# Kernel optimization log

Hardware: AMD Instinct MI355X
Metric: run time of the kernel (lower is better)

Reference implementation:

```python
import jax, jax.numpy as jnp
import numpy as np

EMBED = 256; DEPTH = 64; DEPTH_START = 1.0
POS_RANGE = (-61.2, -61.2, -10.0, 61.2, 61.2, 10.0)
PC_RANGE = (-51.2, -51.2, -5.0, 51.2, 51.2, 3.0)
MEM_LEN = 512; TOPK = 256; NUM_Q = 900; NUM_CLS = 10; CODE = 10; L = 6
B, N, H, W = 4, 6, 16, 44
PAD_H, PAD_W = 256, 704
TWO_PI = 2.0 * np.pi


def _posemb(coords, nf=128):
    # sine/cosine embedding per coordinate channel -> [..., C, nf]
    dim_t = 10000.0 ** (2.0 * (jnp.arange(nf, dtype=jnp.float32) // 2) / nf)
    p = (coords * TWO_PI)[..., None] / dim_t
    p = jnp.stack([jnp.sin(p[..., 0::2]), jnp.cos(p[..., 1::2])], -1)
    return p.reshape(p.shape[:-2] + (nf,))


def _mlp2(x, W1, b1, W2, b2):
    return jnp.maximum(x @ W1 + b1, 0.0) @ W2 + b2


def _conv1x1(x, Wt, b):
    return jnp.einsum('bchw,co->bohw', x, Wt) + b[None, :, None, None]


def _ln(x, g, b):
    m = jnp.mean(x, -1, keepdims=True)
    v = jnp.mean(jnp.square(x - m), -1, keepdims=True)
    return (x - m) / jnp.sqrt(v + 1e-5) * g + b


def _sine_pe(not_mask):
    # SinePositionalEncoding2D, normalize=True; not_mask: [BN,H,W] float
    nf = EMBED // 2; eps = 1e-6
    y = jnp.cumsum(not_mask, 1); x = jnp.cumsum(not_mask, 2)
    y = y / (y[:, -1:, :] + eps) * TWO_PI
    x = x / (x[:, :, -1:] + eps) * TWO_PI
    dim_t = 10000.0 ** (2.0 * (jnp.arange(nf, dtype=jnp.float32) // 2) / nf)
    px = x[..., None] / dim_t; py = y[..., None] / dim_t
    px = jnp.stack([jnp.sin(px[..., 0::2]), jnp.cos(px[..., 1::2])], -1).reshape(x.shape + (nf,))
    py = jnp.stack([jnp.sin(py[..., 0::2]), jnp.cos(py[..., 1::2])], -1).reshape(y.shape + (nf,))
    return jnp.concatenate([py, px], -1).transpose(0, 3, 1, 2)  # [BN,EMBED,H,W]


def _forward(feat, lidar2img, prev_exists, memory_embedding, memory_reference_point,
             memory_timestamp, outs_dec, ref_pts, ip_w, ip_b, pe_w1, pe_b1, pe_w2, pe_b2,
             ap_w1, ap_b1, ap_w2, ap_b2, qe_w1, qe_b1, qe_w2, qe_b2, te_w1, te_b1, te_w2,
             te_b2, cls_w1, cls_b1, cls_g1, cls_be1, cls_w2, cls_b2, cls_g2, cls_be2,
             cls_w3, cls_b3, reg_w1, reg_b1, reg_w2, reg_b2, reg_w3, reg_b3, masks):
    b, n, c, h, w = feat.shape
    # --- pre_update_memory: memory_refresh + timestamp advance ---
    prev = prev_exists.reshape(b, 1, 1)
    mem_e = memory_embedding * prev
    mem_r = memory_reference_point * prev
    mem_t = memory_timestamp * prev + prev
    # --- input projection (1x1 conv) ---
    x = _conv1x1(feat.reshape(b * n, c, h, w), ip_w, ip_b).reshape(b, n, EMBED, h, w)
    # --- 3D position embedding (PETR frustum) ---
    coords_h = jnp.arange(h, dtype=jnp.float32) * (float(PAD_H) / h)
    coords_w = jnp.arange(w, dtype=jnp.float32) * (float(PAD_W) / w)
    d = jnp.arange(DEPTH, dtype=jnp.float32)
    bin_size = (POS_RANGE[3] - DEPTH_START) / (DEPTH * (1.0 + DEPTH))
    coords_d = DEPTH_START + bin_size * d * (d + 1.0)  # LID discretization
    cw, ch_, cd = jnp.meshgrid(coords_w, coords_h, coords_d, indexing='ij')  # [W,H,D]
    xy = jnp.stack([cw, ch_], -1) * jnp.maximum(cd, 1e-5)[..., None]
    coords4 = jnp.concatenate([xy, cd[..., None], jnp.ones_like(cd[..., None])], -1)  # [W,H,D,4]
    img2lidars = jnp.linalg.inv(lidar2img)  # [B,N,4,4]
    c3 = jnp.einsum('bnij,whdj->bnwhdi', img2lidars, coords4)[..., :3]  # [B,N,W,H,D,3]
    lo = jnp.asarray(POS_RANGE[:3], jnp.float32); hi = jnp.asarray(POS_RANGE[3:], jnp.float32)
    c3 = (c3 - lo) / (hi - lo)
    cmask = ((c3 > 1.0) | (c3 < 0.0)).reshape(b, n, w, h, DEPTH * 3).sum(-1) > DEPTH * 0.5
    coords_mask = masks | cmask.transpose(0, 1, 3, 2)
    c3 = c3.transpose(0, 1, 4, 5, 3, 2).reshape(b * n, DEPTH * 3, h, w)
    c3 = jnp.clip(c3, 0.0, 1.0)
    c3 = jnp.log(jnp.clip(c3, 1e-5, None) / jnp.clip(1.0 - c3, 1e-5, None))  # inverse_sigmoid
    coords_pos = _conv1x1(jnp.maximum(_conv1x1(c3, pe_w1, pe_b1), 0.0), pe_w2, pe_b2)
    coords_pos = coords_pos.reshape(b, n, EMBED, h, w)
    # --- 2D sine PE + adapt_pos3d ---
    sine = _sine_pe((~masks).astype(jnp.float32).reshape(b * n, h, w))
    sine = _conv1x1(jnp.maximum(_conv1x1(sine, ap_w1, ap_b1), 0.0), ap_w2, ap_b2)
    pos_embed = coords_pos + sine.reshape(b, n, EMBED, h, w)
    # --- query / time embeddings ---
    qp = _posemb(ref_pts)  # [Q,3,128]
    qp = jnp.concatenate([qp[:, 1], qp[:, 0], qp[:, 2]], -1)  # (y,x,z) -> [Q,384]
    query_pos = _mlp2(qp, qe_w1, qe_b1, qe_w2, qe_b2)  # [Q,256]
    tp = _posemb(mem_t)[..., 0, :]  # [B,M,128]
    time_emb = _mlp2(tp, te_w1, te_b1, te_w2, te_b2)  # [B,M,256]
    # --- cls / reg branches, stacked over decoder layers ---
    hc = jnp.maximum(_ln(jnp.einsum('lbqd,lde->lbqe', outs_dec, cls_w1) + cls_b1[:, None, None], cls_g1[:, None, None], cls_be1[:, None, None]), 0.0)
    hc = jnp.maximum(_ln(jnp.einsum('lbqd,lde->lbqe', hc, cls_w2) + cls_b2[:, None, None], cls_g2[:, None, None], cls_be2[:, None, None]), 0.0)
    all_cls = jnp.einsum('lbqd,ldc->lbqc', hc, cls_w3) + cls_b3[:, None, None]
    hr = jnp.maximum(jnp.einsum('lbqd,lde->lbqe', outs_dec, reg_w1) + reg_b1[:, None, None], 0.0)
    hr = jnp.maximum(jnp.einsum('lbqd,lde->lbqe', hr, reg_w2) + reg_b2[:, None, None], 0.0)
    all_reg = jnp.einsum('lbqd,ldc->lbqc', hr, reg_w3) + reg_b3[:, None, None]
    # --- post_update_memory: sigmoid + topk + gather + rolling concat ---
    rec_score = jnp.max(jax.nn.sigmoid(all_cls[-1]), -1)  # topk(1) over classes == max
    _, idx = jax.lax.top_k(rec_score, TOPK)  # [B,K]
    rec_mem = jax.lax.stop_gradient(jnp.take_along_axis(outs_dec[-1], idx[..., None], axis=1))
    rec_ref = jax.lax.stop_gradient(jnp.take_along_axis(all_reg[-1][..., :3], idx[..., None], axis=1))
    pmin = jnp.asarray(PC_RANGE[:3], jnp.float32); pmax = jnp.asarray(PC_RANGE[3:], jnp.float32)
    rec_ref = jnp.clip((rec_ref - pmin) / jnp.clip(pmax - pmin, 1e-5, None), 0.0, 1.0)
    rec_ts = jnp.zeros((b, TOPK, 1), rec_mem.dtype)
    new_mem_e = jnp.concatenate([rec_mem, mem_e], 1)[:, :MEM_LEN]
    new_mem_r = jnp.concatenate([rec_ref, mem_r], 1)[:, :MEM_LEN]
    new_mem_t = jnp.concatenate([rec_ts, mem_t], 1)[:, :MEM_LEN]
    return (all_cls, all_reg, new_mem_e, new_mem_r, new_mem_t, pos_embed, x, query_pos, time_emb, coords_mask)


def setup_inputs() -> dict:
    key = jax.random.key(0)
    ks = jax.random.split(key, 24)
    def rn(k, shape, s=0.02):
        return jax.random.normal(k, shape, jnp.float32) * s
    inp = dict(
        feat=jax.random.normal(ks[0], (B, N, 256, H, W), jnp.float32),
        lidar2img=jnp.eye(4, dtype=jnp.float32) + 0.05 * jax.random.normal(ks[1], (B, N, 4, 4), jnp.float32),
        prev_exists=jnp.array([1.0, 0.0, 1.0, 1.0], jnp.float32),
        memory_embedding=jax.random.normal(ks[2], (B, MEM_LEN, EMBED), jnp.float32),
        memory_reference_point=jax.random.uniform(ks[3], (B, MEM_LEN, 3)),
        memory_timestamp=jax.random.uniform(ks[4], (B, MEM_LEN, 1)),
        outs_dec=jax.random.normal(ks[5], (L, B, NUM_Q, EMBED), jnp.float32),
        ref_pts=jax.random.uniform(ks[6], (NUM_Q, 3)),
        ip_w=rn(ks[7], (256, EMBED)), ip_b=jnp.zeros(EMBED),
        pe_w1=rn(ks[8], (3 * DEPTH, EMBED * 2)), pe_b1=jnp.zeros(EMBED * 2),
        pe_w2=rn(ks[9], (EMBED * 2, EMBED)), pe_b2=jnp.zeros(EMBED),
        ap_w1=rn(ks[10], (EMBED, EMBED)), ap_b1=jnp.zeros(EMBED),
        ap_w2=rn(ks[11], (EMBED, EMBED)), ap_b2=jnp.zeros(EMBED),
        qe_w1=rn(ks[12], (EMBED * 3 // 2, EMBED)), qe_b1=jnp.zeros(EMBED),
        qe_w2=rn(ks[13], (EMBED, EMBED)), qe_b2=jnp.zeros(EMBED),
        te_w1=rn(ks[14], (EMBED // 2, EMBED)), te_b1=jnp.zeros(EMBED),
        te_w2=rn(ks[15], (EMBED, EMBED)), te_b2=jnp.zeros(EMBED),
        cls_w1=rn(ks[16], (L, EMBED, EMBED)), cls_b1=jnp.zeros((L, EMBED)),
        cls_g1=jnp.ones((L, EMBED)), cls_be1=jnp.zeros((L, EMBED)),
        cls_w2=rn(ks[17], (L, EMBED, EMBED)), cls_b2=jnp.zeros((L, EMBED)),
        cls_g2=jnp.ones((L, EMBED)), cls_be2=jnp.zeros((L, EMBED)),
        cls_w3=rn(ks[18], (L, EMBED, NUM_CLS)), cls_b3=jnp.zeros((L, NUM_CLS)),
        reg_w1=rn(ks[19], (L, EMBED, EMBED)), reg_b1=jnp.zeros((L, EMBED)),
        reg_w2=rn(ks[20], (L, EMBED, EMBED)), reg_b2=jnp.zeros((L, EMBED)),
        reg_w3=rn(ks[21], (L, EMBED, CODE)), reg_b3=jnp.zeros((L, CODE)),
        masks=jnp.zeros((B, N, H, W), bool),
    )
    return inp


def reference(feat, lidar2img, prev_exists, memory_embedding, memory_reference_point,
              memory_timestamp, outs_dec, ref_pts, ip_w, ip_b, pe_w1, pe_b1, pe_w2, pe_b2,
              ap_w1, ap_b1, ap_w2, ap_b2, qe_w1, qe_b1, qe_w2, qe_b2, te_w1, te_b1, te_w2,
              te_b2, cls_w1, cls_b1, cls_g1, cls_be1, cls_w2, cls_b2, cls_g2, cls_be2,
              cls_w3, cls_b3, reg_w1, reg_b1, reg_w2, reg_b2, reg_w3, reg_b3, masks):
    return _forward(feat, lidar2img, prev_exists, memory_embedding, memory_reference_point,
                    memory_timestamp, outs_dec, ref_pts, ip_w, ip_b, pe_w1, pe_b1, pe_w2, pe_b2,
                    ap_w1, ap_b1, ap_w2, ap_b2, qe_w1, qe_b1, qe_w2, qe_b2, te_w1, te_b1, te_w2,
                    te_b2, cls_w1, cls_b1, cls_g1, cls_be1, cls_w2, cls_b2, cls_g2, cls_be2,
                    cls_w3, cls_b3, reg_w1, reg_b1, reg_w2, reg_b2, reg_w3, reg_b3, masks)
```

## Files before the change

### kernel.cpp

```cpp
#include <hip/hip_runtime.h>
#include <math.h>


typedef unsigned short u16;
typedef __attribute__((ext_vector_type(8))) short short8v;
typedef __attribute__((ext_vector_type(4))) float f32x4;

#define DI __device__ __forceinline__
DI u16 f2bf(float f) {
    unsigned x = __float_as_uint(f);
    return (u16)((x + 0x7fffu + ((x >> 16) & 1u)) >> 16);
}
DI float bf2f(u16 u) { return __uint_as_float(((unsigned)u) << 16); }

#define TWO_PI_F 6.283185307179586f

__global__ __launch_bounds__(256) void k_pesrc(
    const float* __restrict__ l2i, u16* __restrict__ c3aT, float* __restrict__ cm,
    float* __restrict__ sineb) {
    int bid = blockIdx.x, tid = threadIdx.x;
    if (bid < 4224) {
        int pix = bid * 4 + (tid >> 6);
        int d = tid & 63;
        int bn = pix / 704, p = pix - bn * 704;
        int h = p / 44, w = p - h * 44;
        const float* Ms = l2i + bn * 16;
        float a[4][8];
#pragma unroll
        for (int i = 0; i < 4; i++)
#pragma unroll
            for (int j = 0; j < 4; j++) {
                a[i][j] = Ms[i * 4 + j];
                a[i][4 + j] = (i == j) ? 1.f : 0.f;
            }
#pragma unroll
        for (int c = 0; c < 4; c++) {
            float ip = 1.f / a[c][c];
#pragma unroll
            for (int j = 0; j < 8; j++) a[c][j] *= ip;
#pragma unroll
            for (int r = 0; r < 4; r++) {
                if (r == c) continue;
                float f = a[r][c];
#pragma unroll
                for (int j = 0; j < 8; j++) a[r][j] -= f * a[c][j];
            }
        }
        float cw = w * 16.0f, ch = h * 16.0f;
        const float bin = (61.2f - 1.0f) / (64.0f * 65.0f);
        float cd = 1.0f + (bin * d) * (d + 1.0f);
        float xx = cw * cd, yy = ch * cd;
        float px = a[0][4] * xx + a[0][5] * yy + a[0][6] * cd + a[0][7];
        float py = a[1][4] * xx + a[1][5] * yy + a[1][6] * cd + a[1][7];
        float pz = a[2][4] * xx + a[2][5] * yy + a[2][6] * cd + a[2][7];
        float c[3];
        c[0] = (px + 61.2f) * (1.f / 122.4f);
        c[1] = (py + 61.2f) * (1.f / 122.4f);
        c[2] = (pz + 10.0f) * (1.f / 20.0f);
        u16* o = c3aT + (size_t)pix * 192 + d * 3;
        int cnt = 0;
#pragma unroll
        for (int i = 0; i < 3; i++) {
            cnt += ((c[i] > 1.0f) || (c[i] < 0.0f)) ? 1 : 0;
            float cc = fminf(fmaxf(c[i], 0.f), 1.f);
            float num = fmaxf(cc, 1e-5f);
            float den = fmaxf(1.0f - cc, 1e-5f);
            o[i] = f2bf(logf(num / den));
        }
        for (int off = 32; off; off >>= 1) cnt += __shfl_down(cnt, off);
        if (d == 0) cm[pix] = (cnt > 32) ? 1.f : 0.f;
    } else {
        int idx = (bid - 4224) * 256 + tid;
        if (idx >= 256 * 704) return;
        int c = idx / 704, p = idx - c * 704;
        int h = p / 44, w = p - h * 44;
        float pos = (c < 128) ? (h + 1) * (TWO_PI_F / (16.0f + 1e-6f))
                              : (w + 1) * (TWO_PI_F / (44.0f + 1e-6f));
        int cc = c & 127, k = cc >> 1;
        float dt = powf(10000.f, k * (1.f / 64.f));
        float arg = pos / dt;
        sineb[idx] = (cc & 1) ? cosf(arg) : sinf(arg);
    }
}

__global__ __launch_bounds__(256) void k_tail(
    const float* __restrict__ memt, const float* __restrict__ prev,
    const float* __restrict__ rp,
    float* __restrict__ fin_t, float* __restrict__ fin_q,
    const float* __restrict__ me, const float* __restrict__ mr,
    float* __restrict__ oe, float* __restrict__ orr, float* __restrict__ ot) {
    int bid = blockIdx.x, tid = threadIdx.x;
    if (bid < 1187) {
        int idx = bid * 256 + tid;
        if (idx < 131072) {
            int row = idx >> 6, p = idx & 63;
            float pv = prev[row >> 9];
            float mt = memt[row] * pv + pv;
            float dt = powf(10000.f, p * (1.f / 64.f));
            float arg = mt * TWO_PI_F / dt;
            float s, c;
            sincosf(arg, &s, &c);
            *(float2*)&fin_t[row * 128 + 2 * p] = make_float2(s, c);
        } else if (idx < 131072 + 172800) {
            int q = idx - 131072;
            int row = q / 192, p = q - row * 192;
            int f = 2 * p, seg = f >> 7, ff = f & 127;
            int cidx = (seg == 0) ? 1 : ((seg == 1) ? 0 : 2);
            float rv = rp[row * 3 + cidx];
            float dt = powf(10000.f, (ff >> 1) * (1.f / 64.f));
            float arg = rv * TWO_PI_F / dt;
            float s, c;
            sincosf(arg, &s, &c);
            *(float2*)&fin_q[row * 384 + f] = make_float2(s, c);
        }
    } else {
        int bb = bid - 1187;
        int b = bb >> 8, j = bb & 255, o = tid;
        float pv = prev[b];
        oe[(size_t)(b * 512 + 256 + j) * 256 + o] = me[(size_t)(b * 512 + j) * 256 + o] * pv;
        if (o < 3)
            orr[(size_t)(b * 512 + 256 + j) * 3 + o] = mr[(size_t)(b * 512 + j) * 3 + o] * pv;
        if (o == 0) {
            ot[b * 512 + 256 + j] = memt[b * 512 + j] * pv + pv;
            ot[b * 512 + j] = 0.f;
        }
    }
}

__global__ __launch_bounds__(256) void k_wtrA(
    const float* __restrict__ cls_w1, const float* __restrict__ reg_w1,
    const float* __restrict__ cls_w2, const float* __restrict__ reg_w2,
    u16* __restrict__ w1Tc, u16* __restrict__ w1Tr,
    u16* __restrict__ w2Tc, u16* __restrict__ w2Tr,
    const float* __restrict__ pe_w1, u16* __restrict__ pe1T,
    const float* __restrict__ pe_w2, u16* __restrict__ pe2T,
    const float* __restrict__ ip_w, u16* __restrict__ ipT,
    const float* __restrict__ ap_w1, u16* __restrict__ ap1T,
    const float* __restrict__ ap_w2, u16* __restrict__ ap2T,
    const float* __restrict__ cls_w3, u16* __restrict__ c3T,
    const float* __restrict__ reg_w3, u16* __restrict__ r3T,
    const float* __restrict__ od, u16* __restrict__ odb) {
    __shared__ float sh[32][33];
    int bid = blockIdx.x;
    if (bid >= 2048) {
        int e0 = (bid - 2048) * 2048 + threadIdx.x * 8;
        int zz = e0 / 921600, rem = e0 - zz * 921600;
        int row = rem >> 8, c = rem & 255;
        const float* src = od + e0;
        float4 f0 = *(const float4*)src;
        float4 f1 = *(const float4*)(src + 4);
        uint4 u;
        u.x = f2bf(f0.x) | ((unsigned)f2bf(f0.y) << 16);
        u.y = f2bf(f0.z) | ((unsigned)f2bf(f0.w) << 16);
        u.z = f2bf(f1.x) | ((unsigned)f2bf(f1.y) << 16);
        u.w = f2bf(f1.z) | ((unsigned)f2bf(f1.w) << 16);
        u16* dst = odb + (size_t)zz * 1867776 +
                   ((size_t)((row >> 6) * 8 + (c >> 5))) * 4096 + (row & 63) * 32 + (c & 31);
        *(uint4*)dst = u;
        return;
    }
    if (bid >= 1952) {
        int r = bid - 1952;
        int ti = r >> 3, k0 = (r & 7) * 32;
        const float* src = (ti < 6) ? cls_w3 + (size_t)ti * 2560
                                    : reg_w3 + (size_t)(ti - 6) * 2560;
        u16* dst = (ti < 6) ? c3T + (size_t)ti * 2560
                            : r3T + (size_t)(ti - 6) * 2560;
        for (int i = threadIdx.x; i < 320; i += 256) {
            int k = i / 10, n = i - (i / 10) * 10;
            dst[n * 256 + k0 + k] = f2bf(src[(size_t)(k0 + k) * 10 + n]);
        }
        return;
    }
    const float* src; u16* dst; int K, N, x, y;
    if (bid < 1536) {
        int x_ = bid & 7, y_ = (bid >> 3) & 7, z = bid >> 6;
        int ti = z / 6, zz = z - ti * 6;
        const float* s = (ti == 0) ? cls_w1 : (ti == 1) ? reg_w1 : (ti == 2) ? cls_w2 : reg_w2;
        u16* dd = (ti == 0) ? w1Tc : (ti == 1) ? w1Tr : (ti == 2) ? w2Tc : w2Tr;
        src = s + (size_t)zz * 65536; dst = dd + (size_t)zz * 65536;
        K = 256; N = 256; x = x_; y = y_;
    } else if (bid < 1632) {
        int r = bid - 1536; x = r & 15; y = r >> 4;
        src = pe_w1; dst = pe1T; K = 192; N = 512;
    } else if (bid < 1760) {
        int r = bid - 1632; x = r & 7; y = r >> 3;
        src = pe_w2; dst = pe2T; K = 512; N = 256;
    } else {
        int r = bid - 1760; x = r & 7; y = (r >> 3) & 7;
        int ti = r >> 6;
        src = (ti == 0) ? ip_w : (ti == 1) ? ap_w1 : ap_w2;
        dst = (ti == 0) ? ipT : (ti == 1) ? ap1T : ap2T;
        K = 256; N = 256;
    }
    int n0 = x * 32, k0 = y * 32;
    int tx = threadIdx.x & 31, ty = threadIdx.x >> 5;
#pragma unroll
    for (int r = 0; r < 4; r++)
        sh[ty + 8 * r][tx] = src[(size_t)(k0 + ty + 8 * r) * N + n0 + tx];
    __syncthreads();
#pragma unroll
    for (int r = 0; r < 4; r++)
        dst[(size_t)(n0 + ty + 8 * r) * K + k0 + tx] = f2bf(sh[tx][ty + 8 * r]);
}

template <int AF32, int BTRANS, int BF32, int OUTF32, int ADD, int BIASM, int APANEL>
__global__ __launch_bounds__(256) void k_mfma(
    const void* __restrict__ Av, const void* __restrict__ B1v, const void* __restrict__ B2v,
    const float* __restrict__ bias1, const float* __restrict__ bias2,
    const float* __restrict__ add, void* __restrict__ outv,
    int M, int N, int K, int lda, int ldb, int ldo,
    long aZ, long bZ, long biasZ, long oZ, int zsplit, int zrelu, int aFull, int zpair) {
    __shared__ __align__(16) u16 As[64][40];
    __shared__ __align__(16) u16 Bs[128][40];
    const int tid = threadIdx.x;
    const int z = blockIdx.z;
    const int half = zpair ? (z & 1) : ((z < zsplit) ? 0 : 1);
    const int zz = zpair ? (z >> 1) : (z - (half ? zsplit : 0));
    const int lz = zpair ? (half * zsplit + zz) : z;
    const void* Bv = half ? B2v : B1v;
    const float* bias = (half ? bias2 : bias1) + (size_t)zz * biasZ;
    const bool relu = zpair ? (half >= zrelu) : (z >= zrelu);
    const long aOff = (long)(aFull ? lz : zz) * aZ;
    const long bOff = (long)zz * bZ;
    const int m0 = blockIdx.y * 64, n0 = blockIdx.x * 128;
    const int wave = tid >> 6, lane = tid & 63, quad = lane >> 4, l16 = lane & 15;
    const int wm = (wave >> 1) * 32, wn = (wave & 1) * 64;
    const int ar = tid >> 2, ak = (tid & 3) << 3;
    const int br = tid & 127, bk = (tid >> 7) << 4;
    f32x4 acc[2][4] = {};

    float pAf[8]; uint4 pAu = make_uint4(0, 0, 0, 0);
    float pBf[16]; u16 pBh[16];
    uint4 pBu0 = make_uint4(0, 0, 0, 0), pBu1 = make_uint4(0, 0, 0, 0);

    auto loadA = [&](int kt) {
        if (APANEL) {
            const u16* ap = (const u16*)Av + aOff +
                            ((size_t)(m0 >> 6) * (K >> 5) + (kt >> 5)) * 4096 + tid * 8;
            pAu = *(const uint4*)ap;
        } else if (AF32) {
            int gm = m0 + ar;
#pragma unroll
            for (int q = 0; q < 8; q++) pAf[q] = 0.f;
            if (gm < M) {
                const float* ap = (const float*)Av + aOff + (size_t)gm * lda + kt + ak;
                float4 f0 = *(const float4*)ap;
                float4 f1 = *(const float4*)(ap + 4);
                pAf[0] = f0.x; pAf[1] = f0.y; pAf[2] = f0.z; pAf[3] = f0.w;
                pAf[4] = f1.x; pAf[5] = f1.y; pAf[6] = f1.z; pAf[7] = f1.w;
            }
        } else {
            int gm = m0 + ar;
            pAu = make_uint4(0, 0, 0, 0);
            if (gm < M)
                pAu = *(const uint4*)((const u16*)Av + aOff + (size_t)gm * lda + kt + ak);
        }
    };
    auto storeA = [&]() {
        if (AF32) {
            uint4 u;
            u.x = f2bf(pAf[0]) | ((unsigned)f2bf(pAf[1]) << 16);
            u.y = f2bf(pAf[2]) | ((unsigned)f2bf(pAf[3]) << 16);
            u.z = f2bf(pAf[4]) | ((unsigned)f2bf(pAf[5]) << 16);
            u.w = f2bf(pAf[6]) | ((unsigned)f2bf(pAf[7]) << 16);
            *(uint4*)&As[ar][ak] = u;
        } else {
            *(uint4*)&As[ar][ak] = pAu;
        }
    };
    auto loadB = [&](int kt) {
        int gn = n0 + br;
        if (!BTRANS) {
            pBu0 = make_uint4(0, 0, 0, 0);
            pBu1 = make_uint4(0, 0, 0, 0);
            if (gn < N) {
                const u16* bp = (const u16*)Bv + bOff + (size_t)gn * ldb + kt + bk;
                pBu0 = *(const uint4*)bp;
                pBu1 = *(const uint4*)(bp + 8);
            }
        } else if (BF32) {
#pragma unroll
            for (int kk = 0; kk < 16; kk++)
                pBf[kk] = (gn < N) ? ((const float*)Bv + bOff)[(size_t)(kt + bk + kk) * ldb + gn]
                                   : 0.f;
        } else {
#pragma unroll
            for (int kk = 0; kk < 16; kk++)
                pBh[kk] = (gn < N) ? ((const u16*)Bv + bOff)[(size_t)(kt + bk + kk) * ldb + gn]
                                   : (u16)0;
        }
    };
    auto storeB = [&]() {
        if (!BTRANS) {
            *(uint4*)&Bs[br][bk] = pBu0;
            *(uint4*)&Bs[br][bk + 8] = pBu1;
        } else {
            u16 t[16];
#pragma unroll
            for (int kk = 0; kk < 16; kk++) t[kk] = BF32 ? f2bf(pBf[kk]) : pBh[kk];
            uint4 u0, u1;
            u0.x = t[0] | ((unsigned)t[1] << 16);
            u0.y = t[2] | ((unsigned)t[3] << 16);
            u0.z = t[4] | ((unsigned)t[5] << 16);
            u0.w = t[6] | ((unsigned)t[7] << 16);
            u1.x = t[8] | ((unsigned)t[9] << 16);
            u1.y = t[10] | ((unsigned)t[11] << 16);
            u1.z = t[12] | ((unsigned)t[13] << 16);
            u1.w = t[14] | ((unsigned)t[15] << 16);
            *(uint4*)&Bs[br][bk] = u0;
            *(uint4*)&Bs[br][bk + 8] = u1;
        }
    };

    loadA(0); loadB(0);
    for (int kt = 0; kt < K; kt += 32) {
        storeA(); storeB();
        __syncthreads();
        if (kt + 32 < K) { loadA(kt + 32); loadB(kt + 32); }
        short8v af[2], bfr[4];
#pragma unroll
        for (int i = 0; i < 2; i++) af[i] = *(const short8v*)&As[wm + i * 16 + l16][quad * 8];
#pragma unroll
        for (int j = 0; j < 4; j++) bfr[j] = *(const short8v*)&Bs[wn + j * 16 + l16][quad * 8];
#pragma unroll
        for (int i = 0; i < 2; i++)
#pragma unroll
            for (int j = 0; j < 4; j++)
                acc[i][j] = __builtin_amdgcn_mfma_f32_16x16x32_bf16(af[i], bfr[j], acc[i][j], 0, 0, 0);
        __syncthreads();
    }

    float* outf = (float*)outv + (size_t)lz * oZ;
    u16* outh = (u16*)outv + (size_t)lz * oZ;
#pragma unroll
    for (int i = 0; i < 2; i++) {
#pragma unroll
        for (int r = 0; r < 4; r++) {
            int row = m0 + wm + i * 16 + quad * 4 + r;
            if (row >= M) continue;
#pragma unroll
            for (int j = 0; j < 4; j++) {
                int col = n0 + wn + j * 16 + l16;
                if (col >= N) continue;
                float v = acc[i][j][r] + (BIASM ? bias[row] : bias[col]);
                if (relu) v = fmaxf(v, 0.f);
                if (ADD) v += add[(size_t)row * ldo + col];
                if (OUTF32) outf[(size_t)row * ldo + col] = v;
                else        outh[(size_t)row * ldo + col] = f2bf(v);
            }
        }
    }
}

template <int RELU>
DI void sgemm_body(const float* __restrict__ A, const float* __restrict__ Bm,
                   const float* __restrict__ bias, float* __restrict__ out,
                   int M, int K, int lda) {
    __shared__ __align__(16) float As[16][68];
    __shared__ __align__(16) float Bs[16][68];
    const int tid = threadIdx.x;
    const int m0 = blockIdx.y * 64, n0 = blockIdx.x * 64;
    const int tm = tid >> 4, tn = tid & 15;
    const int kA = tid >> 4, mA = (tid << 2) & 63;
    const int mN = tid & 63, kq = tid >> 6;
    float acc[4][4] = {};
    for (int kt = 0; kt < K; kt += 16) {
        int gm = m0 + mN;
        float4 u = {0.f, 0.f, 0.f, 0.f};
        if (gm < M) u = *(const float4*)(A + (size_t)gm * lda + kt + (kq << 2));
        As[(kq << 2) + 0][mN] = u.x; As[(kq << 2) + 1][mN] = u.y;
        As[(kq << 2) + 2][mN] = u.z; As[(kq << 2) + 3][mN] = u.w;
        {
            float4 b = *(const float4*)(Bm + (size_t)(kt + kA) * 256 + n0 + mA);
            Bs[kA][mA + 0] = b.x; Bs[kA][mA + 1] = b.y;
            Bs[kA][mA + 2] = b.z; Bs[kA][mA + 3] = b.w;
        }
        __syncthreads();
#pragma unroll
        for (int k = 0; k < 16; k++) {
            const float4 av = *(const float4*)(&As[k][tm << 2]);
            const float4 bv = *(const float4*)(&Bs[k][tn << 2]);
            float ar[4] = {av.x, av.y, av.z, av.w};
            float br[4] = {bv.x, bv.y, bv.z, bv.w};
#pragma unroll
            for (int i = 0; i < 4; i++)
#pragma unroll
                for (int j = 0; j < 4; j++) acc[i][j] = fmaf(ar[i], br[j], acc[i][j]);
        }
        __syncthreads();
    }
#pragma unroll
    for (int i = 0; i < 4; i++) {
        int row = m0 + (tm << 2) + i;
        if (row >= M) continue;
        float4 o4;
        o4.x = acc[i][0] + bias[n0 + (tn << 2) + 0];
        o4.y = acc[i][1] + bias[n0 + (tn << 2) + 1];
        o4.z = acc[i][2] + bias[n0 + (tn << 2) + 2];
        o4.w = acc[i][3] + bias[n0 + (tn << 2) + 3];
        if (RELU) {
            o4.x = fmaxf(o4.x, 0.f); o4.y = fmaxf(o4.y, 0.f);
            o4.z = fmaxf(o4.z, 0.f); o4.w = fmaxf(o4.w, 0.f);
        }
        *(float4*)(out + (size_t)row * 256 + n0 + (tn << 2)) = o4;
    }
}

template <int RELU>
__global__ __launch_bounds__(256) void k_sgemm2(
    const float* __restrict__ A, const float* __restrict__ Bm,
    const float* __restrict__ bias, float* __restrict__ out,
    int M, int K, int lda) {
    sgemm_body<RELU>(A, Bm, bias, out, M, K, lda);
}

template <int RELU>
__global__ __launch_bounds__(256) void k_sgemm3(
    const float* __restrict__ A0, const float* __restrict__ B0,
    const float* __restrict__ b0, float* __restrict__ o0, int M0, int K0, int lda0,
    const float* __restrict__ A1, const float* __restrict__ B1,
    const float* __restrict__ b1, float* __restrict__ o1, int M1, int K1, int lda1) {
    const float* A; const float* Bm; const float* bias; float* out; int M, K, lda;
    if (blockIdx.z == 0) { A = A0; Bm = B0; bias = b0; out = o0; M = M0; K = K0; lda = lda0; }
    else                 { A = A1; Bm = B1; bias = b1; out = o1; M = M1; K = K1; lda = lda1; }
    if ((int)blockIdx.y * 64 >= M) return;
    sgemm_body<RELU>(A, Bm, bias, out, M, K, lda);
}

__global__ __launch_bounds__(256) void k_lnb(
    u16* __restrict__ buf, const float* __restrict__ g, const float* __restrict__ be) {
    int tid = threadIdx.x, wid = tid >> 6, lane = tid & 63;
    int row = blockIdx.x * 4 + wid;
    int l = row / 3600;
    size_t base = (size_t)row * 256 + lane;
    float v[4];
#pragma unroll
    for (int i = 0; i < 4; i++) v[i] = bf2f(buf[base + (i << 6)]);
    float s = v[0] + v[1] + v[2] + v[3];
    for (int off = 32; off; off >>= 1) s += __shfl_down(s, off);
    s = __shfl(s, 0);
    float mean = s * (1.f / 256.f);
    float d[4], q = 0.f;
#pragma unroll
    for (int i = 0; i < 4; i++) { d[i] = v[i] - mean; q += d[i] * d[i]; }
    for (int off = 32; off; off >>= 1) q += __shfl_down(q, off);
    q = __shfl(q, 0);
    float rstd = rsqrtf(q * (1.f / 256.f) + 1e-5f);
#pragma unroll
    for (int i = 0; i < 4; i++) {
        int c = lane + (i << 6);
        buf[base + (i << 6)] = f2bf(fmaxf(d[i] * rstd * g[l * 256 + c] + be[l * 256 + c], 0.f));
    }
}

__global__ __launch_bounds__(256) void k_ln5(
    float* __restrict__ buf, const float* __restrict__ g, const float* __restrict__ be) {
    int tid = threadIdx.x, wid = tid >> 6, lane = tid & 63;
    int row = blockIdx.x * 4 + wid;
    size_t base = (size_t)row * 256 + lane;
    float v[4];
#pragma unroll
    for (int i = 0; i < 4; i++) v[i] = buf[base + (i << 6)];
    float s = v[0] + v[1] + v[2] + v[3];
    for (int off = 32; off; off >>= 1) s += __shfl_down(s, off);
    s = __shfl(s, 0);
    float mean = s * (1.f / 256.f);
    float d[4], q = 0.f;
#pragma unroll
    for (int i = 0; i < 4; i++) { d[i] = v[i] - mean; q += d[i] * d[i]; }
    for (int off = 32; off; off >>= 1) q += __shfl_down(q, off);
    q = __shfl(q, 0);
    float rstd = rsqrtf(q * (1.f / 256.f) + 1e-5f);
#pragma unroll
    for (int i = 0; i < 4; i++) {
        int c = lane + (i << 6);
        buf[base + (i << 6)] = fmaxf(d[i] * rstd * g[c] + be[c], 0.f);
    }
}

__global__ __launch_bounds__(320) void k_score(
    const float* __restrict__ h2, const float* __restrict__ wc, const float* __restrict__ bc,
    float* __restrict__ score) {
    __shared__ float sh[32][256];
    __shared__ float clsv[32][10];
    int tb = blockIdx.x * 32, tid = threadIdx.x;
    for (int i = tid; i < 8192; i += 320) {
        int rr = i >> 8, k = i & 255;
        int tok = tb + rr;
        sh[rr][k] = (tok < 3600) ? h2[(size_t)tok * 256 + k] : 0.f;
    }
    __syncthreads();
    int tl = tid / 10, o = tid - tl * 10;
    const float* w = wc + 5 * 2560 + o;
    float ac = 0.f;
    for (int k = 0; k < 256; k++) ac += sh[tl][k] * w[k * 10];
    ac += bc[5 * 10 + o];
    int tok = tb + tl;
    if (tok < 3600) clsv[tl][o] = ac;
    __syncthreads();
    if (tid < 32 && tb + tid < 3600) {
        float m = clsv[tid][0];
#pragma unroll
        for (int c = 1; c < 10; c++) m = fmaxf(m, clsv[tid][c]);
        score[tb + tid] = m;
    }
}

__global__ __launch_bounds__(1024) void k_sel(
    const float* __restrict__ score, int* __restrict__ sel) {
    __shared__ float sc[900];
    int b = blockIdx.x, tid = threadIdx.x;
    for (int i = tid; i < 900; i += 1024) sc[i] = score[b * 900 + i];
    __syncthreads();
    if (tid < 900) {
        float s = sc[tid];
        int r = 0;
        for (int j = 0; j < 900; j++) {
            float sj = sc[j];
            r += ((sj > s) || (sj == s && j < tid)) ? 1 : 0;
        }
        if (r < 256) sel[b * 256 + r] = tid;
    }
}

__global__ __launch_bounds__(256) void k_gather(
    const int* __restrict__ sel, const float* __restrict__ oreg,
    const float* __restrict__ od, float* __restrict__ oe, float* __restrict__ orr) {
    int b = blockIdx.y;
    int r = blockIdx.x * 4 + (threadIdx.x >> 6);
    int lane = threadIdx.x & 63;
    int q = sel[b * 256 + r];
    const float4* src = (const float4*)(od + (size_t)((20 + b) * 900 + q) * 256);
    float4* dst = (float4*)(oe + (size_t)(b * 512 + r) * 256);
    dst[lane] = src[lane];
    if (lane == 0) {
#pragma unroll
        for (int kk = 0; kk < 3; kk++) {
            float v = oreg[(size_t)(5 * 3600 + b * 900 + q) * 10 + kk];
            float lo = (kk == 2) ? -5.0f : -51.2f;
            float rng = (kk == 2) ? 8.0f : 102.4f;
            orr[(size_t)(b * 512 + r) * 3 + kk] = fminf(fmaxf((v - lo) / rng, 0.f), 1.f);
        }
    }
}

extern "C" void kernel_launch(void* const* d_in, const int* in_sizes, int n_in,
                              void* d_out, int out_size, void* d_ws, size_t ws_size,
                              hipStream_t stream) {
    const float* feat   = (const float*)d_in[0];
    const float* l2i    = (const float*)d_in[1];
    const float* prev   = (const float*)d_in[2];
    const float* meme   = (const float*)d_in[3];
    const float* memr   = (const float*)d_in[4];
    const float* memt   = (const float*)d_in[5];
    const float* od     = (const float*)d_in[6];
    const float* rp     = (const float*)d_in[7];
    const float* ip_w   = (const float*)d_in[8];
    const float* ip_b   = (const float*)d_in[9];
    const float* pe_w1  = (const float*)d_in[10];
    const float* pe_b1  = (const float*)d_in[11];
    const float* pe_w2  = (const float*)d_in[12];
    const float* pe_b2  = (const float*)d_in[13];
    const float* ap_w1  = (const float*)d_in[14];
    const float* ap_b1  = (const float*)d_in[15];
    const float* ap_w2  = (const float*)d_in[16];
    const float* ap_b2  = (const float*)d_in[17];
    const float* qe_w1  = (const float*)d_in[18];
    const float* qe_b1  = (const float*)d_in[19];
    const float* qe_w2  = (const float*)d_in[20];
    const float* qe_b2  = (const float*)d_in[21];
    const float* te_w1  = (const float*)d_in[22];
    const float* te_b1  = (const float*)d_in[23];
    const float* te_w2  = (const float*)d_in[24];
    const float* te_b2  = (const float*)d_in[25];
    const float* cls_w1 = (const float*)d_in[26];
    const float* cls_b1 = (const float*)d_in[27];
    const float* cls_g1 = (const float*)d_in[28];
    const float* cls_be1= (const float*)d_in[29];
    const float* cls_w2 = (const float*)d_in[30];
    const float* cls_b2 = (const float*)d_in[31];
    const float* cls_g2 = (const float*)d_in[32];
    const float* cls_be2= (const float*)d_in[33];
    const float* cls_w3 = (const float*)d_in[34];
    const float* cls_b3 = (const float*)d_in[35];
    const float* reg_w1 = (const float*)d_in[36];
    const float* reg_b1 = (const float*)d_in[37];
    const float* reg_w2 = (const float*)d_in[38];
    const float* reg_b2 = (const float*)d_in[39];
    const float* reg_w3 = (const float*)d_in[40];
    const float* reg_b3 = (const float*)d_in[41];

    float* o32    = (float*)d_out;
    float* o_cls  = o32;
    float* o_reg  = o32 + 216000;
    float* o_meme = o32 + 432000;
    float* o_memr = o32 + 956288;
    float* o_memt = o32 + 962432;
    float* o_pos  = o32 + 964480;
    float* o_x    = o32 + 5289856;
    float* o_qp   = o32 + 9615232;
    float* o_te   = o32 + 9845632;
    float* o_cm   = o32 + 10369920;

    u16*   w1Tc = (u16*)(o32 + 5961600);
    u16*   w1Tr = (u16*)(o32 + 6158208);
    u16*   w2Tc = (u16*)(o32 + 6354816);
    u16*   w2Tr = (u16*)(o32 + 6551424);
    float* h1f  = o32 + 432000;
    float* h2f  = o32 + 1353600;
    u16*   c3aT = (u16*)(o32 + 964480);
    float* sineb = o32 + 432000;
    float* sinea = o32 + 612224;
    u16*   hapb  = (u16*)(o32 + 792448);
    u16*   h1pe  = (u16*)(o32 + 5289856);
    u16*   pe1T  = (u16*)(o32 + 9615232);
    u16*   pe2T  = (u16*)(o32 + 9664384);
    u16*   ap1T  = (u16*)(o32 + 9729920);
    u16*   ap2T  = (u16*)(o32 + 9762688);
    float* w_score = o32 + 9845632;
    int*   w_sel   = (int*)(o32 + 9860416);
    u16*   ipT     = (u16*)(o32 + 9861440);
    u16*   c3T     = (u16*)(o32 + 9894208);
    u16*   r3T     = (u16*)(o32 + 9901888);

    float* ws    = (float*)d_ws;
    float* fin_t = ws;
    float* h1_t  = ws + 262144;
    float* fin_q = ws + 786432;
    float* h1_q  = ws + 1132032;
    u16*   h1d   = (u16*)(ws + 1400000);
    u16*   h2d   = (u16*)(ws + 7000000);
    u16*   odb   = (u16*)(ws + 12600000);

    k_wtrA<<<4748, 256, 0, stream>>>(cls_w1, reg_w1, cls_w2, reg_w2,
                                     w1Tc, w1Tr, w2Tc, w2Tr,
                                     pe_w1, pe1T, pe_w2, pe2T,
                                     ip_w, ipT, ap_w1, ap1T, ap_w2, ap2T,
                                     cls_w3, c3T, reg_w3, r3T,
                                     od, odb);

    k_mfma<0, 0, 0, 0, 0, 0, 1><<<dim3(2, 57, 12), 256, 0, stream>>>(
        odb, w1Tc, w1Tr, cls_b1, reg_b1, nullptr, h1d,
        3600, 256, 256, 256, 256, 256, 1867776, 65536, 256, 921600, 6, 1, 0, 1);
    k_lnb<<<5400, 256, 0, stream>>>(h1d, cls_g1, cls_be1);
    k_mfma<0, 0, 0, 0, 0, 0, 0><<<dim3(2, 57, 12), 256, 0, stream>>>(
        h1d, w2Tc, w2Tr, cls_b2, reg_b2, nullptr, h2d,
        3600, 256, 256, 256, 256, 256, 921600, 65536, 256, 921600, 6, 6, 1, 0);
    k_lnb<<<5400, 256, 0, stream>>>(h2d, cls_g2, cls_be2);
    k_mfma<0, 0, 0, 1, 0, 0, 0><<<dim3(1, 57, 12), 256, 0, stream>>>(
        h2d, c3T, r3T, cls_b3, reg_b3, nullptr, o_cls,
        3600, 10, 256, 256, 256, 10, 921600, 2560, 10, 36000, 6, 99, 1, 0);

    k_sgemm2<0><<<dim3(4, 57), 256, 0, stream>>>(od + (size_t)5 * 921600, cls_w1 + 5 * 65536,
                                                 cls_b1 + 5 * 256, h1f, 3600, 256, 256);
    k_ln5<<<900, 256, 0, stream>>>(h1f, cls_g1 + 5 * 256, cls_be1 + 5 * 256);
    k_sgemm2<0><<<dim3(4, 57), 256, 0, stream>>>(h1f, cls_w2 + 5 * 65536, cls_b2 + 5 * 256,
                                                 h2f, 3600, 256, 256);
    k_ln5<<<900, 256, 0, stream>>>(h2f, cls_g2 + 5 * 256, cls_be2 + 5 * 256);
    k_score<<<113, 320, 0, stream>>>(h2f, cls_w3, cls_b3, w_score);

    k_pesrc<<<4928, 256, 0, stream>>>(l2i, c3aT, o_cm, sineb);
    k_mfma<0, 1, 1, 0, 0, 1, 0><<<dim3(6, 4, 1), 256, 0, stream>>>(
        ap1T, sineb, sineb, ap_b1, ap_b1, nullptr, hapb,
        256, 704, 256, 256, 704, 704, 0, 0, 0, 0, 99, 0, 0, 0);
    k_mfma<0, 1, 0, 1, 0, 1, 0><<<dim3(6, 4, 1), 256, 0, stream>>>(
        ap2T, hapb, hapb, ap_b2, ap_b2, nullptr, sinea,
        256, 704, 256, 256, 704, 704, 0, 0, 0, 0, 99, 99, 0, 0);
    k_mfma<0, 0, 0, 0, 0, 1, 0><<<dim3(6, 8, 24), 256, 0, stream>>>(
        pe1T, c3aT, c3aT, pe_b1, pe_b1, nullptr, h1pe,
        512, 704, 192, 192, 192, 704, 0, 135168, 0, 360448, 99, 0, 0, 0);
    k_mfma<0, 1, 0, 1, 1, 1, 0><<<dim3(6, 4, 24), 256, 0, stream>>>(
        pe2T, h1pe, h1pe, pe_b2, pe_b2, sinea, o_pos,
        256, 704, 512, 512, 704, 704, 0, 360448, 0, 180224, 99, 99, 0, 0);
    k_mfma<0, 1, 1, 1, 0, 1, 0><<<dim3(6, 4, 24), 256, 0, stream>>>(
        ipT, feat, feat, ip_b, ip_b, nullptr, o_x,
        256, 704, 256, 256, 704, 704, 0, 180224, 0, 180224, 99, 99, 0, 0);

    k_sel<<<4, 1024, 0, stream>>>(w_score, w_sel);
    k_gather<<<dim3(64, 4), 256, 0, stream>>>(w_sel, o_reg, od, o_meme, o_memr);

    k_tail<<<2211, 256, 0, stream>>>(memt, prev, rp, fin_t, fin_q,
                                     meme, memr, o_meme, o_memr, o_memt);
    k_sgemm3<1><<<dim3(4, 32, 2), 256, 0, stream>>>(
        fin_t, te_w1, te_b1, h1_t, 2048, 128, 128,
        fin_q, qe_w1, qe_b1, h1_q, 900, 384, 384);
    k_sgemm3<0><<<dim3(4, 32, 2), 256, 0, stream>>>(
        h1_t, te_w2, te_b2, o_te, 2048, 256, 256,
        h1_q, qe_w2, qe_b2, o_qp, 900, 256, 256);
}
```

Baseline: 519.3 us.

## Store classifier/regressor hidden activations in 64x32 panel layout across MLP chain

Hidden activations h1d and h2d of the cls/reg MLPs now use a tiled 64-row by 32-column panel layout. The GEMMs write this layout directly, the layernorm kernel reads and writes it, and the next GEMM loads its A tiles as contiguous 16-byte chunks. The panel stride is also fixed so that 32-wide panels pack densely. The aim is coalesced, bounds-check-free A loads in the second and third GEMMs, in exchange for scattered 2-byte stores in the epilogue and strided layernorm accesses.

```diff
diff --git a/kernel.cpp b/kernel.cpp
--- a/kernel.cpp
+++ b/kernel.cpp
@@ -14,6 +14,7 @@
 DI float bf2f(u16 u) { return __uint_as_float(((unsigned)u) << 16); }
 
 #define TWO_PI_F 6.283185307179586f
+#define PSLOT 933888
 
 __global__ __launch_bounds__(256) void k_pesrc(
     const float* __restrict__ l2i, u16* __restrict__ c3aT, float* __restrict__ cm,
@@ -154,8 +155,8 @@
         u.y = f2bf(f0.z) | ((unsigned)f2bf(f0.w) << 16);
         u.z = f2bf(f1.x) | ((unsigned)f2bf(f1.y) << 16);
         u.w = f2bf(f1.z) | ((unsigned)f2bf(f1.w) << 16);
-        u16* dst = odb + (size_t)zz * 1867776 +
-                   ((size_t)((row >> 6) * 8 + (c >> 5))) * 4096 + (row & 63) * 32 + (c & 31);
+        u16* dst = odb + (size_t)zz * PSLOT +
+                   ((size_t)((row >> 6) * 8 + (c >> 5))) * 2048 + (row & 63) * 32 + (c & 31);
         *(uint4*)dst = u;
         return;
     }
@@ -204,7 +205,7 @@
         dst[(size_t)(n0 + ty + 8 * r) * K + k0 + tx] = f2bf(sh[tx][ty + 8 * r]);
 }
 
-template <int AF32, int BTRANS, int BF32, int OUTF32, int ADD, int BIASM, int APANEL>
+template <int AF32, int BTRANS, int BF32, int OUTF32, int ADD, int BIASM, int APANEL, int OPANEL>
 __global__ __launch_bounds__(256) void k_mfma(
     const void* __restrict__ Av, const void* __restrict__ B1v, const void* __restrict__ B2v,
     const float* __restrict__ bias1, const float* __restrict__ bias2,
@@ -237,7 +238,7 @@
     auto loadA = [&](int kt) {
         if (APANEL) {
             const u16* ap = (const u16*)Av + aOff +
-                            ((size_t)(m0 >> 6) * (K >> 5) + (kt >> 5)) * 4096 + tid * 8;
+                            ((size_t)(m0 >> 6) * (K >> 5) + (kt >> 5)) * 2048 + tid * 8;
             pAu = *(const uint4*)ap;
         } else if (AF32) {
             int gm = m0 + ar;
@@ -346,8 +347,11 @@
                 float v = acc[i][j][r] + (BIASM ? bias[row] : bias[col]);
                 if (relu) v = fmaxf(v, 0.f);
                 if (ADD) v += add[(size_t)row * ldo + col];
-                if (OUTF32) outf[(size_t)row * ldo + col] = v;
-                else        outh[(size_t)row * ldo + col] = f2bf(v);
+                if (OPANEL)
+                    outh[((size_t)(row >> 6) * (ldo >> 5) + (col >> 5)) * 2048 +
+                         (row & 63) * 32 + (col & 31)] = f2bf(v);
+                else if (OUTF32) outf[(size_t)row * ldo + col] = v;
+                else             outh[(size_t)row * ldo + col] = f2bf(v);
             }
         }
     }
@@ -428,15 +432,18 @@
     sgemm_body<RELU>(A, Bm, bias, out, M, K, lda);
 }
 
-__global__ __launch_bounds__(256) void k_lnb(
+__global__ __launch_bounds__(256) void k_lnbp(
     u16* __restrict__ buf, const float* __restrict__ g, const float* __restrict__ be) {
     int tid = threadIdx.x, wid = tid >> 6, lane = tid & 63;
-    int row = blockIdx.x * 4 + wid;
-    int l = row / 3600;
-    size_t base = (size_t)row * 256 + lane;
+    int R = blockIdx.x * 4 + wid;
+    int l = R / 3600, r = R - l * 3600;
+    u16* base = buf + (size_t)l * PSLOT + (size_t)(r >> 6) * 8 * 2048 + (r & 63) * 32;
     float v[4];
 #pragma unroll
-    for (int i = 0; i < 4; i++) v[i] = bf2f(buf[base + (i << 6)]);
+    for (int i = 0; i < 4; i++) {
+        int c = lane + (i << 6);
+        v[i] = bf2f(base[(c >> 5) * 2048 + (c & 31)]);
+    }
     float s = v[0] + v[1] + v[2] + v[3];
     for (int off = 32; off; off >>= 1) s += __shfl_down(s, off);
     s = __shfl(s, 0);
@@ -450,7 +457,8 @@
 #pragma unroll
     for (int i = 0; i < 4; i++) {
         int c = lane + (i << 6);
-        buf[base + (i << 6)] = f2bf(fmaxf(d[i] * rstd * g[l * 256 + c] + be[l * 256 + c], 0.f));
+        base[(c >> 5) * 2048 + (c & 31)] =
+            f2bf(fmaxf(d[i] * rstd * g[l * 256 + c] + be[l * 256 + c], 0.f));
     }
 }
 
@@ -630,8 +638,8 @@
     float* fin_q = ws + 786432;
     float* h1_q  = ws + 1132032;
     u16*   h1d   = (u16*)(ws + 1400000);
-    u16*   h2d   = (u16*)(ws + 7000000);
-    u16*   odb   = (u16*)(ws + 12600000);
+    u16*   h2d   = (u16*)(ws + 7100000);
+    u16*   odb   = (u16*)(ws + 12800000);
 
     k_wtrA<<<4748, 256, 0, stream>>>(cls_w1, reg_w1, cls_w2, reg_w2,
                                      w1Tc, w1Tr, w2Tc, w2Tr,
@@ -640,17 +648,17 @@
                                      cls_w3, c3T, reg_w3, r3T,
                                      od, odb);
 
-    k_mfma<0, 0, 0, 0, 0, 0, 1><<<dim3(2, 57, 12), 256, 0, stream>>>(
+    k_mfma<0, 0, 0, 0, 0, 0, 1, 1><<<dim3(2, 57, 12), 256, 0, stream>>>(
         odb, w1Tc, w1Tr, cls_b1, reg_b1, nullptr, h1d,
-        3600, 256, 256, 256, 256, 256, 1867776, 65536, 256, 921600, 6, 1, 0, 1);
-    k_lnb<<<5400, 256, 0, stream>>>(h1d, cls_g1, cls_be1);
-    k_mfma<0, 0, 0, 0, 0, 0, 0><<<dim3(2, 57, 12), 256, 0, stream>>>(
+        3600, 256, 256, 256, 256, 256, PSLOT, 65536, 256, PSLOT, 6, 1, 0, 1);
+    k_lnbp<<<5400, 256, 0, stream>>>(h1d, cls_g1, cls_be1);
+    k_mfma<0, 0, 0, 0, 0, 0, 1, 1><<<dim3(2, 57, 12), 256, 0, stream>>>(
         h1d, w2Tc, w2Tr, cls_b2, reg_b2, nullptr, h2d,
-        3600, 256, 256, 256, 256, 256, 921600, 65536, 256, 921600, 6, 6, 1, 0);
-    k_lnb<<<5400, 256, 0, stream>>>(h2d, cls_g2, cls_be2);
-    k_mfma<0, 0, 0, 1, 0, 0, 0><<<dim3(1, 57, 12), 256, 0, stream>>>(
+        3600, 256, 256, 256, 256, 256, PSLOT, 65536, 256, PSLOT, 6, 6, 1, 0);
+    k_lnbp<<<5400, 256, 0, stream>>>(h2d, cls_g2, cls_be2);
+    k_mfma<0, 0, 0, 1, 0, 0, 1, 0><<<dim3(1, 57, 12), 256, 0, stream>>>(
         h2d, c3T, r3T, cls_b3, reg_b3, nullptr, o_cls,
-        3600, 10, 256, 256, 256, 10, 921600, 2560, 10, 36000, 6, 99, 1, 0);
+        3600, 10, 256, 256, 256, 10, PSLOT, 2560, 10, 36000, 6, 99, 1, 0);
 
     k_sgemm2<0><<<dim3(4, 57), 256, 0, stream>>>(od + (size_t)5 * 921600, cls_w1 + 5 * 65536,
                                                  cls_b1 + 5 * 256, h1f, 3600, 256, 256);
@@ -661,19 +669,19 @@
     k_score<<<113, 320, 0, stream>>>(h2f, cls_w3, cls_b3, w_score);
 
     k_pesrc<<<4928, 256, 0, stream>>>(l2i, c3aT, o_cm, sineb);
-    k_mfma<0, 1, 1, 0, 0, 1, 0><<<dim3(6, 4, 1), 256, 0, stream>>>(
+    k_mfma<0, 1, 1, 0, 0, 1, 0, 0><<<dim3(6, 4, 1), 256, 0, stream>>>(
         ap1T, sineb, sineb, ap_b1, ap_b1, nullptr, hapb,
         256, 704, 256, 256, 704, 704, 0, 0, 0, 0, 99, 0, 0, 0);
-    k_mfma<0, 1, 0, 1, 0, 1, 0><<<dim3(6, 4, 1), 256, 0, stream>>>(
+    k_mfma<0, 1, 0, 1, 0, 1, 0, 0><<<dim3(6, 4, 1), 256, 0, stream>>>(
         ap2T, hapb, hapb, ap_b2, ap_b2, nullptr, sinea,
         256, 704, 256, 256, 704, 704, 0, 0, 0, 0, 99, 99, 0, 0);
-    k_mfma<0, 0, 0, 0, 0, 1, 0><<<dim3(6, 8, 24), 256, 0, stream>>>(
+    k_mfma<0, 0, 0, 0, 0, 1, 0, 0><<<dim3(6, 8, 24), 256, 0, stream>>>(
         pe1T, c3aT, c3aT, pe_b1, pe_b1, nullptr, h1pe,
         512, 704, 192, 192, 192, 704, 0, 135168, 0, 360448, 99, 0, 0, 0);
-    k_mfma<0, 1, 0, 1, 1, 1, 0><<<dim3(6, 4, 24), 256, 0, stream>>>(
+    k_mfma<0, 1, 0, 1, 1, 1, 0, 0><<<dim3(6, 4, 24), 256, 0, stream>>>(
         pe2T, h1pe, h1pe, pe_b2, pe_b2, sinea, o_pos,
         256, 704, 512, 512, 704, 704, 0, 360448, 0, 180224, 99, 99, 0, 0);
-    k_mfma<0, 1, 1, 1, 0, 1, 0><<<dim3(6, 4, 24), 256, 0, stream>>>(
+    k_mfma<0, 1, 1, 1, 0, 1, 0, 0><<<dim3(6, 4, 24), 256, 0, stream>>>(
         ipT, feat, feat, ip_b, ip_b, nullptr, o_x,
         256, 704, 256, 256, 704, 704, 0, 180224, 0, 180224, 99, 99, 0, 0);
 
```

After: 504.9 us. 2.8% less time.
